# Performance work log

Measured on AMD Instinct MI355X. Metric: run time of the kernel, lower is better.

The kernel has to match this reference:

```python
import jax, jax.numpy as jnp
import numpy as np

C = 512
C8 = C // 8   # query/key dim = 64
C2 = C // 2   # value dim = 256


def setup_inputs() -> dict:
    key = jax.random.key(0)
    ks = jax.random.split(key, 10)
    B, H, W = 4, 64, 64
    x = jax.random.normal(ks[0], (B, H, W, C), dtype=jnp.float32)
    # 1x1 conv kernels expressed as [in_ch, out_ch] matrices + biases
    Wf = jax.random.normal(ks[1], (C, C8), dtype=jnp.float32) * 0.02
    bf = jnp.zeros((C8,), dtype=jnp.float32)
    Wg = jax.random.normal(ks[2], (C, C8), dtype=jnp.float32) * 0.02
    bg = jnp.zeros((C8,), dtype=jnp.float32)
    Wh = jax.random.normal(ks[3], (C, C2), dtype=jnp.float32) * 0.02
    bh = jnp.zeros((C2,), dtype=jnp.float32)
    Wo = jax.random.normal(ks[4], (C2, C), dtype=jnp.float32) * 0.02
    bo = jnp.zeros((C,), dtype=jnp.float32)
    gamma = jax.random.normal(ks[5], (1,), dtype=jnp.float32) * 0.05
    return {"x": x, "Wf": Wf, "bf": bf, "Wg": Wg, "bg": bg,
            "Wh": Wh, "bh": bh, "Wo": Wo, "bo": bo, "gamma": gamma}


def reference(x, Wf, bf, Wg, bg, Wh, bh, Wo, bo, gamma):
    B, H, W, _ = x.shape
    N = H * W
    xf = x.reshape(B, N, C)                               # flatten spatial dims
    f = xf @ Wf + bf                                      # [B, N, C8] keys
    g = xf @ Wg + bg                                      # [B, N, C8] queries
    h = xf @ Wh + bh                                      # [B, N, C2] values
    s = jnp.einsum('bnd,bmd->bnm', g, f)                  # [B, N, N] scores (g @ f^T)
    beta = jax.nn.softmax(s, axis=-1)                     # attention map
    o = jnp.einsum('bnm,bmd->bnd', beta, h)               # [B, N, C2]
    o = o @ Wo + bo                                       # [B, N, C] output 1x1 conv
    out = gamma * o + xf                                  # residual with learned scale
    return out.reshape(B, H, W, C)
```

## Files before the change

kernel.cpp:

```cpp
#include <hip/hip_runtime.h>
#include <math.h>

#define B_   4
#define N_   4096
#define C_   512
#define C8_  64
#define C2_  256
#define LOG2E 1.4426950408889634f

typedef __attribute__((ext_vector_type(8))) short bf16x8;
typedef __attribute__((ext_vector_type(4))) short bf16x4;
typedef __attribute__((ext_vector_type(4))) float floatx4;
typedef __attribute__((ext_vector_type(16))) float floatx16;
typedef __attribute__((ext_vector_type(2))) unsigned uint32x2;

__device__ __forceinline__ short f2bf(float x) {
    unsigned u = __float_as_uint(x);
    u += 0x7fff + ((u >> 16) & 1);
    return (short)(u >> 16);
}
__device__ __forceinline__ unsigned cvtpk(float a, float b) {
    unsigned r;
    asm("v_cvt_pk_bf16_f32 %0, %1, %2" : "=v"(r) : "v"(a), "v"(b));
    return r;
}
__device__ __forceinline__ float bf2f(short s) {
    return __uint_as_float(((unsigned)(unsigned short)s) << 16);
}

union U8 { bf16x8 v; unsigned u[4]; };
union U4 { bf16x4 v; unsigned u[2]; };

__global__ __launch_bounds__(256) void convert_w(
    const float* __restrict__ Wf, const float* __restrict__ Wg,
    const float* __restrict__ Wh, const float* __restrict__ Wo,
    short* __restrict__ WcatT, short* __restrict__ WoT)
{
    int tid = blockIdx.x * 256 + threadIdx.x;
    if (tid < 384 * 512) {
        int n = tid >> 9, k = tid & 511;
        float v = (n < 64)  ? Wf[k * 64 + n]
                : (n < 128) ? Wg[k * 64 + (n - 64)]
                            : Wh[k * 256 + (n - 128)];
        WcatT[tid] = f2bf(v);
    } else {
        int t2 = tid - 384 * 512;
        int n = t2 >> 8, k = t2 & 255;
        WoT[t2] = f2bf(Wo[k * 512 + n]);
    }
}

__global__ __launch_bounds__(256, 3) void qkv_mfma(
    const float* __restrict__ x, const short* __restrict__ WcatT,
    const float* __restrict__ bfv, const float* __restrict__ bgv,
    const float* __restrict__ bhv,
    short* __restrict__ fbf, short* __restrict__ gbf, short* __restrict__ hT)
{
    const int ny = blockIdx.x;
    const int m0 = blockIdx.y * 64;
    const int n0 = ny * 128;
    const int t  = threadIdx.x;
    const int w  = t >> 6, lane = t & 63;
    const int l15 = lane & 15, quad = lane >> 4;
    const int wm = w & 1, wn = w >> 1;

    __shared__ short As[64 * 40];
    __shared__ short Bs[128 * 40];

    const int arow = t >> 2, ako = (t & 3) * 8;

    floatx4 acc[2][4];
    #pragma unroll
    for (int i = 0; i < 2; i++)
        #pragma unroll
        for (int j = 0; j < 4; j++) acc[i][j] = (floatx4){0.f,0.f,0.f,0.f};

    for (int k0 = 0; k0 < C_; k0 += 32) {
        {
            const float* xp = &x[(size_t)(m0 + arow) * C_ + k0 + ako];
            float4 v0 = *(const float4*)xp;
            float4 v1 = *(const float4*)(xp + 4);
            U8 ua;
            ua.u[0] = cvtpk(v0.x, v0.y); ua.u[1] = cvtpk(v0.z, v0.w);
            ua.u[2] = cvtpk(v1.x, v1.y); ua.u[3] = cvtpk(v1.z, v1.w);
            *(bf16x8*)&As[arow * 40 + ako] = ua.v;
        }
        #pragma unroll
        for (int i = 0; i < 2; i++) {
            int c = t + i * 256;
            int nr = c >> 2, ko = (c & 3) * 8;
            *(bf16x8*)&Bs[nr * 40 + ko] =
                *(const bf16x8*)&WcatT[(size_t)(n0 + nr) * 512 + k0 + ko];
        }
        __syncthreads();

        bf16x8 af[2], bfr[4];
        #pragma unroll
        for (int mt = 0; mt < 2; mt++)
            af[mt] = *(const bf16x8*)&As[(wm * 32 + mt * 16 + l15) * 40 + quad * 8];
        #pragma unroll
        for (int nt = 0; nt < 4; nt++)
            bfr[nt] = *(const bf16x8*)&Bs[(wn * 64 + nt * 16 + l15) * 40 + quad * 8];
        #pragma unroll
        for (int mt = 0; mt < 2; mt++)
            #pragma unroll
            for (int nt = 0; nt < 4; nt++)
                acc[mt][nt] = __builtin_amdgcn_mfma_f32_16x16x32_bf16(af[mt], bfr[nt], acc[mt][nt], 0, 0, 0);
        __syncthreads();
    }

    if (ny == 0) {
        #pragma unroll
        for (int mt = 0; mt < 2; mt++) {
            #pragma unroll
            for (int nt = 0; nt < 4; nt++) {
                int cn = wn * 64 + nt * 16 + l15;
                #pragma unroll
                for (int rg = 0; rg < 4; rg++) {
                    int row = m0 + wm * 32 + mt * 16 + quad * 4 + rg;
                    float v = acc[mt][nt][rg];
                    if (cn < 64) fbf[(size_t)row * 64 + cn]        = f2bf(v + bfv[cn]);
                    else         gbf[(size_t)row * 64 + (cn - 64)] = f2bf((v + bgv[cn - 64]) * LOG2E);
                }
            }
        }
    } else {
        #pragma unroll
        for (int mt = 0; mt < 2; mt++) {
            #pragma unroll
            for (int nt = 0; nt < 4; nt++) {
                int hch = (ny - 1) * 128 + wn * 64 + nt * 16 + l15;
                int row = m0 + wm * 32 + mt * 16 + quad * 4;
                int bb = row >> 12, n = row & 4095;
                float bias = bhv[hch];
                U4 pk;
                pk.u[0] = cvtpk(acc[mt][nt][0] + bias, acc[mt][nt][1] + bias);
                pk.u[1] = cvtpk(acc[mt][nt][2] + bias, acc[mt][nt][3] + bias);
                *(bf16x4*)&hT[((size_t)(bb * 256 + hch)) * 4096 + n] = pk.v;
            }
        }
    }
}

#define HST 40

__global__ __launch_bounds__(256, 2) void attn_v6(
    const short* __restrict__ fK,
    const short* __restrict__ gQ,
    const short* __restrict__ hT,
    short* __restrict__ oPart,
    float* __restrict__ lPart,
    int sbits)
{
    const int bx = blockIdx.x;
    const int s  = bx & ((1 << sbits) - 1);
    const int vh = (bx >> sbits) & 1;
    const int qt = (bx >> (sbits + 1)) & 31;
    const int b  = bx >> (sbits + 6);
    const int kb = s << (12 - sbits);
    const int niter = 64 >> sbits;
    const int t  = threadIdx.x;
    const int w  = t >> 6, lane = t & 63;
    const int l31 = lane & 31, h = lane >> 5;
    const int q_wave = qt * 128 + w * 32;

    __shared__ short fs[2][64 * HST];
    __shared__ short hs[2][128 * HST];

    bf16x8 qf[4];
    #pragma unroll
    for (int k = 0; k < 4; k++)
        qf[k] = *(const bf16x8*)&gQ[(size_t)(b * N_ + q_wave + l31) * 64 + k * 16 + h * 8];

    floatx16 oacc[4];
    #pragma unroll
    for (int vt = 0; vt < 4; vt++)
        #pragma unroll
        for (int j = 0; j < 16; j++) oacc[vt][j] = 0.f;
    float lsum = 0.f;

    const int f_row = t >> 2, f_c = (t & 3) * 16;
    const int h_row = t >> 3, h_c = (t & 7) * 8;

    {
        *(bf16x8*)&fs[0][f_row * HST + f_c] =
            *(const bf16x8*)&fK[(size_t)(b * N_ + kb + f_row) * 64 + f_c];
        *(bf16x8*)&fs[0][f_row * HST + f_c + 8] =
            *(const bf16x8*)&fK[(size_t)(b * N_ + kb + f_row) * 64 + f_c + 8];
        #pragma unroll
        for (int i = 0; i < 4; i++)
            *(bf16x8*)&hs[0][(h_row + i * 32) * HST + h_c] =
                *(const bf16x8*)&hT[((size_t)(b * 256 + vh * 128 + h_row + i * 32)) * 4096 + kb + h_c];
    }
    __syncthreads();

    for (int it = 0; it < niter; ++it) {
        const int cur = it & 1;
        const bool more = (it < niter - 1);
        const int kn = kb + (it + 1) * 64;

        bf16x8 rf0, rf1, rh[4];
        if (more) {
            rf0 = *(const bf16x8*)&fK[(size_t)(b * N_ + kn + f_row) * 64 + f_c];
            rf1 = *(const bf16x8*)&fK[(size_t)(b * N_ + kn + f_row) * 64 + f_c + 8];
            #pragma unroll
            for (int i = 0; i < 4; i++)
                rh[i] = *(const bf16x8*)&hT[((size_t)(b * 256 + vh * 128 + h_row + i * 32)) * 4096 + kn + h_c];
        }

        bf16x8 ffr[2][4];
        #pragma unroll
        for (int m = 0; m < 2; m++)
            #pragma unroll
            for (int k = 0; k < 4; k++)
                ffr[m][k] = *(const bf16x8*)&fs[cur][(m * 32 + l31) * HST + k * 16 + h * 8];

        floatx16 sacc[2];
        __builtin_amdgcn_s_setprio(1);
        #pragma unroll
        for (int m = 0; m < 2; m++) {
            #pragma unroll
            for (int j = 0; j < 16; j++) sacc[m][j] = 0.f;
            #pragma unroll
            for (int k = 0; k < 4; k++)
                sacc[m] = __builtin_amdgcn_mfma_f32_32x32x16_bf16(
                    ffr[m][k], qf[k], sacc[m], 0, 0, 0);
        }
        __builtin_amdgcn_s_setprio(0);

        bf16x8 pfrag[4];
        #pragma unroll
        for (int m = 0; m < 2; m++) {
            float p[16]; float ps_ = 0.f;
            #pragma unroll
            for (int j = 0; j < 16; j++) {
                p[j] = __builtin_amdgcn_exp2f(sacc[m][j]);
                ps_ += p[j];
            }
            ps_ += __shfl_xor(ps_, 32);
            lsum += ps_;
            unsigned pk[8];
            #pragma unroll
            for (int i = 0; i < 8; i++) pk[i] = cvtpk(p[2 * i], p[2 * i + 1]);
            #pragma unroll
            for (int kp = 0; kp < 2; kp++) {
                uint32x2 r0 = __builtin_amdgcn_permlane32_swap(pk[4 * kp],     pk[4 * kp + 2], false, false);
                uint32x2 r1 = __builtin_amdgcn_permlane32_swap(pk[4 * kp + 1], pk[4 * kp + 3], false, false);
                U8 u; u.u[0] = r0[0]; u.u[1] = r1[0]; u.u[2] = r0[1]; u.u[3] = r1[1];
                pfrag[m * 2 + kp] = u.v;
            }
        }

        __builtin_amdgcn_s_setprio(1);
        #pragma unroll
        for (int kk2 = 0; kk2 < 4; kk2++)
            #pragma unroll
            for (int vt = 0; vt < 4; vt++) {
                bf16x8 vfr = *(const bf16x8*)&hs[cur][(vt * 32 + l31) * HST + kk2 * 16 + h * 8];
                oacc[vt] = __builtin_amdgcn_mfma_f32_32x32x16_bf16(
                    pfrag[kk2], vfr, oacc[vt], 0, 0, 0);
            }
        __builtin_amdgcn_s_setprio(0);

        if (more) {
            const int nxt = cur ^ 1;
            *(bf16x8*)&fs[nxt][f_row * HST + f_c] = rf0;
            *(bf16x8*)&fs[nxt][f_row * HST + f_c + 8] = rf1;
            #pragma unroll
            for (int i = 0; i < 4; i++)
                *(bf16x8*)&hs[nxt][(h_row + i * 32) * HST + h_c] = rh[i];
        }
        __syncthreads();
    }

    #pragma unroll
    for (int vt = 0; vt < 4; vt++) {
        int vch = vh * 128 + vt * 32 + l31;
        #pragma unroll
        for (int r = 0; r < 16; r++) {
            int q = q_wave + (r & 3) + 8 * (r >> 2) + 4 * h;
            oPart[(size_t)s * 4194304 + (size_t)(b * N_ + q) * 256 + vch] = f2bf(oacc[vt][r]);
        }
    }
    if (vh == 0 && lane < 32)
        lPart[(size_t)s * 16384 + b * N_ + q_wave + lane] = lsum;
}

__global__ __launch_bounds__(256, 2) void out_mfma(
    const short* __restrict__ oPart, const float* __restrict__ lPart,
    const short* __restrict__ WoT,
    const float* __restrict__ bo, const float* __restrict__ x,
    const float* __restrict__ gamma, float* __restrict__ out)
{
    const int n0 = blockIdx.x * 256;
    const int m0 = blockIdx.y * 64;
    const int t  = threadIdx.x;
    const int w  = t >> 6, lane = t & 63;
    const int l15 = lane & 15, quad = lane >> 4;
    const int wm = w & 1, wn = w >> 1;

    __shared__ short As[64 * 40];
    __shared__ short Bs[256 * 40];
    __shared__ float linv[64];

    if (t < 64)
        linv[t] = 1.0f / (lPart[m0 + t] + lPart[16384 + m0 + t]);

    const int arow = t >> 2, ako = (t & 3) * 8;

    floatx4 acc[2][8];
    #pragma unroll
    for (int i = 0; i < 2; i++)
        #pragma unroll
        for (int j = 0; j < 8; j++) acc[i][j] = (floatx4){0.f,0.f,0.f,0.f};

    __syncthreads();

    for (int k0 = 0; k0 < C2_; k0 += 32) {
        {
            size_t gb = (size_t)(m0 + arow) * 256 + k0 + ako;
            bf16x8 o0 = *(const bf16x8*)&oPart[gb];
            bf16x8 o1 = *(const bf16x8*)&oPart[4194304 + gb];
            float li = linv[arow];
            U8 u;
            #pragma unroll
            for (int j = 0; j < 4; j++) {
                float a0 = (bf2f(o0[2 * j])     + bf2f(o1[2 * j]))     * li;
                float a1 = (bf2f(o0[2 * j + 1]) + bf2f(o1[2 * j + 1])) * li;
                u.u[j] = cvtpk(a0, a1);
            }
            *(bf16x8*)&As[arow * 40 + ako] = u.v;
        }
        #pragma unroll
        for (int i = 0; i < 4; i++) {
            int c = t + i * 256;
            int nr = c >> 2, ko = (c & 3) * 8;
            *(bf16x8*)&Bs[nr * 40 + ko] =
                *(const bf16x8*)&WoT[(size_t)(n0 + nr) * 256 + k0 + ko];
        }
        __syncthreads();

        bf16x8 af[2], bfr[8];
        #pragma unroll
        for (int mt = 0; mt < 2; mt++)
            af[mt] = *(const bf16x8*)&As[(wm * 32 + mt * 16 + l15) * 40 + quad * 8];
        #pragma unroll
        for (int nt = 0; nt < 8; nt++)
            bfr[nt] = *(const bf16x8*)&Bs[(wn * 128 + nt * 16 + l15) * 40 + quad * 8];
        #pragma unroll
        for (int mt = 0; mt < 2; mt++)
            #pragma unroll
            for (int nt = 0; nt < 8; nt++)
                acc[mt][nt] = __builtin_amdgcn_mfma_f32_16x16x32_bf16(af[mt], bfr[nt], acc[mt][nt], 0, 0, 0);
        __syncthreads();
    }

    const float gm = gamma[0];
    #pragma unroll
    for (int mt = 0; mt < 2; mt++) {
        #pragma unroll
        for (int nt = 0; nt < 8; nt++) {
            int col = n0 + wn * 128 + nt * 16 + l15;
            float bias = bo[col];
            #pragma unroll
            for (int rg = 0; rg < 4; rg++) {
                int row = m0 + wm * 32 + mt * 16 + quad * 4 + rg;
                out[(size_t)row * C_ + col] =
                    gm * (acc[mt][nt][rg] + bias) + x[(size_t)row * C_ + col];
            }
        }
    }
}

extern "C" void kernel_launch(void* const* d_in, const int* in_sizes, int n_in,
                              void* d_out, int out_size, void* d_ws, size_t ws_size,
                              hipStream_t stream) {
    (void)in_sizes; (void)n_in; (void)out_size; (void)ws_size;

    const float* x     = (const float*)d_in[0];
    const float* Wf    = (const float*)d_in[1];
    const float* bfv   = (const float*)d_in[2];
    const float* Wg    = (const float*)d_in[3];
    const float* bgv   = (const float*)d_in[4];
    const float* Wh    = (const float*)d_in[5];
    const float* bhv   = (const float*)d_in[6];
    const float* Wo    = (const float*)d_in[7];
    const float* bo    = (const float*)d_in[8];
    const float* gamma = (const float*)d_in[9];
    float* out = (float*)d_out;

    short* fbf   = (short*)d_ws;
    short* gbf   = fbf   + (size_t)B_ * N_ * C8_;
    short* hT    = gbf   + (size_t)B_ * N_ * C8_;
    short* WcatT = hT    + (size_t)B_ * C2_ * N_;
    short* WoT   = WcatT + (size_t)384 * 512;
    short* oPart = WoT   + (size_t)512 * 256;
    float* lPart = (float*)(oPart + (size_t)2 * 16384 * 256);

    const int sbits = 1;

    convert_w<<<1280, 256, 0, stream>>>(Wf, Wg, Wh, Wo, WcatT, WoT);
    qkv_mfma<<<dim3(3, 256), 256, 0, stream>>>(x, WcatT, bfv, bgv, bhv, fbf, gbf, hT);
    attn_v6<<<256 << sbits, 256, 0, stream>>>(fbf, gbf, hT, oPart, lPart, sbits);
    out_mfma<<<dim3(2, 256), 256, 0, stream>>>(oPart, lPart, WoT, bo, x, gamma, out);
}
```

Before: 194.4 us.

## Single-buffer attention LDS, raise occupancy, and split keys four ways

The attention kernel drops the double-buffered LDS (the two buffer slots are reused as the two halves of the key dimension) and adds an extra barrier before the shared-memory writes. It also restructures the score loop to process one 32-row block at a time so fewer registers are live, and raises launch bounds to 3 blocks per CU. The key-split factor goes from 2 to 4, and the output projection now sums a variable number of partial outputs and row sums. This trades lost load/compute overlap and a second barrier per iteration for higher occupancy and more blocks, while the output kernel reads twice as much partial data.

```diff
diff --git a/kernel.cpp b/kernel.cpp
--- a/kernel.cpp
+++ b/kernel.cpp
@@ -143,8 +143,10 @@
 }
 
 #define HST 40
-
-__global__ __launch_bounds__(256, 2) void attn_v6(
+#define FS_H (64 * HST + 32)
+#define HS_H (128 * HST + 32)
+
+__global__ __launch_bounds__(256, 3) void attn_v9(
     const short* __restrict__ fK,
     const short* __restrict__ gQ,
     const short* __restrict__ hT,
@@ -164,8 +166,8 @@
     const int l31 = lane & 31, h = lane >> 5;
     const int q_wave = qt * 128 + w * 32;
 
-    __shared__ short fs[2][64 * HST];
-    __shared__ short hs[2][128 * HST];
+    __shared__ short fs[2][FS_H];
+    __shared__ short hs[2][HS_H];
 
     bf16x8 qf[4];
     #pragma unroll
@@ -180,22 +182,23 @@
     float lsum = 0.f;
 
     const int f_row = t >> 2, f_c = (t & 3) * 16;
+    const int fh = f_c >> 5, fw = f_c & 31;
     const int h_row = t >> 3, h_c = (t & 7) * 8;
+    const int hh = h_c >> 5, hw = h_c & 31;
 
     {
-        *(bf16x8*)&fs[0][f_row * HST + f_c] =
+        *(bf16x8*)&fs[fh][f_row * HST + fw] =
             *(const bf16x8*)&fK[(size_t)(b * N_ + kb + f_row) * 64 + f_c];
-        *(bf16x8*)&fs[0][f_row * HST + f_c + 8] =
+        *(bf16x8*)&fs[fh][f_row * HST + fw + 8] =
             *(const bf16x8*)&fK[(size_t)(b * N_ + kb + f_row) * 64 + f_c + 8];
         #pragma unroll
         for (int i = 0; i < 4; i++)
-            *(bf16x8*)&hs[0][(h_row + i * 32) * HST + h_c] =
+            *(bf16x8*)&hs[hh][(h_row + i * 32) * HST + hw] =
                 *(const bf16x8*)&hT[((size_t)(b * 256 + vh * 128 + h_row + i * 32)) * 4096 + kb + h_c];
     }
     __syncthreads();
 
     for (int it = 0; it < niter; ++it) {
-        const int cur = it & 1;
         const bool more = (it < niter - 1);
         const int kn = kb + (it + 1) * 64;
 
@@ -208,33 +211,27 @@
                 rh[i] = *(const bf16x8*)&hT[((size_t)(b * 256 + vh * 128 + h_row + i * 32)) * 4096 + kn + h_c];
         }
 
-        bf16x8 ffr[2][4];
-        #pragma unroll
-        for (int m = 0; m < 2; m++)
+        bf16x8 pfrag[4];
+        #pragma unroll
+        for (int m = 0; m < 2; m++) {
+            bf16x8 ffr[4];
             #pragma unroll
             for (int k = 0; k < 4; k++)
-                ffr[m][k] = *(const bf16x8*)&fs[cur][(m * 32 + l31) * HST + k * 16 + h * 8];
-
-        floatx16 sacc[2];
-        __builtin_amdgcn_s_setprio(1);
-        #pragma unroll
-        for (int m = 0; m < 2; m++) {
-            #pragma unroll
-            for (int j = 0; j < 16; j++) sacc[m][j] = 0.f;
+                ffr[k] = *(const bf16x8*)&fs[k >> 1][(m * 32 + l31) * HST + (k & 1) * 16 + h * 8];
+
+            floatx16 sacc;
+            #pragma unroll
+            for (int j = 0; j < 16; j++) sacc[j] = 0.f;
+            __builtin_amdgcn_s_setprio(1);
             #pragma unroll
             for (int k = 0; k < 4; k++)
-                sacc[m] = __builtin_amdgcn_mfma_f32_32x32x16_bf16(
-                    ffr[m][k], qf[k], sacc[m], 0, 0, 0);
-        }
-        __builtin_amdgcn_s_setprio(0);
-
-        bf16x8 pfrag[4];
-        #pragma unroll
-        for (int m = 0; m < 2; m++) {
+                sacc = __builtin_amdgcn_mfma_f32_32x32x16_bf16(ffr[k], qf[k], sacc, 0, 0, 0);
+            __builtin_amdgcn_s_setprio(0);
+
             float p[16]; float ps_ = 0.f;
             #pragma unroll
             for (int j = 0; j < 16; j++) {
-                p[j] = __builtin_amdgcn_exp2f(sacc[m][j]);
+                p[j] = __builtin_amdgcn_exp2f(sacc[j]);
                 ps_ += p[j];
             }
             ps_ += __shfl_xor(ps_, 32);
@@ -256,21 +253,21 @@
         for (int kk2 = 0; kk2 < 4; kk2++)
             #pragma unroll
             for (int vt = 0; vt < 4; vt++) {
-                bf16x8 vfr = *(const bf16x8*)&hs[cur][(vt * 32 + l31) * HST + kk2 * 16 + h * 8];
+                bf16x8 vfr = *(const bf16x8*)&hs[kk2 >> 1][(vt * 32 + l31) * HST + (kk2 & 1) * 16 + h * 8];
                 oacc[vt] = __builtin_amdgcn_mfma_f32_32x32x16_bf16(
                     pfrag[kk2], vfr, oacc[vt], 0, 0, 0);
             }
         __builtin_amdgcn_s_setprio(0);
 
+        __syncthreads();
         if (more) {
-            const int nxt = cur ^ 1;
-            *(bf16x8*)&fs[nxt][f_row * HST + f_c] = rf0;
-            *(bf16x8*)&fs[nxt][f_row * HST + f_c + 8] = rf1;
+            *(bf16x8*)&fs[fh][f_row * HST + fw] = rf0;
+            *(bf16x8*)&fs[fh][f_row * HST + fw + 8] = rf1;
             #pragma unroll
             for (int i = 0; i < 4; i++)
-                *(bf16x8*)&hs[nxt][(h_row + i * 32) * HST + h_c] = rh[i];
-        }
-        __syncthreads();
+                *(bf16x8*)&hs[hh][(h_row + i * 32) * HST + hw] = rh[i];
+            __syncthreads();
+        }
     }
 
     #pragma unroll
@@ -290,7 +287,8 @@
     const short* __restrict__ oPart, const float* __restrict__ lPart,
     const short* __restrict__ WoT,
     const float* __restrict__ bo, const float* __restrict__ x,
-    const float* __restrict__ gamma, float* __restrict__ out)
+    const float* __restrict__ gamma, float* __restrict__ out,
+    int nsplit)
 {
     const int n0 = blockIdx.x * 256;
     const int m0 = blockIdx.y * 64;
@@ -303,8 +301,11 @@
     __shared__ short Bs[256 * 40];
     __shared__ float linv[64];
 
-    if (t < 64)
-        linv[t] = 1.0f / (lPart[m0 + t] + lPart[16384 + m0 + t]);
+    if (t < 64) {
+        float l = 0.f;
+        for (int s2 = 0; s2 < nsplit; s2++) l += lPart[(size_t)s2 * 16384 + m0 + t];
+        linv[t] = 1.0f / l;
+    }
 
     const int arow = t >> 2, ako = (t & 3) * 8;
 
@@ -319,16 +320,19 @@
     for (int k0 = 0; k0 < C2_; k0 += 32) {
         {
             size_t gb = (size_t)(m0 + arow) * 256 + k0 + ako;
-            bf16x8 o0 = *(const bf16x8*)&oPart[gb];
-            bf16x8 o1 = *(const bf16x8*)&oPart[4194304 + gb];
+            float a[8];
+            #pragma unroll
+            for (int j = 0; j < 8; j++) a[j] = 0.f;
+            for (int s2 = 0; s2 < nsplit; s2++) {
+                bf16x8 o = *(const bf16x8*)&oPart[(size_t)s2 * 4194304 + gb];
+                #pragma unroll
+                for (int j = 0; j < 8; j++) a[j] += bf2f(o[j]);
+            }
             float li = linv[arow];
             U8 u;
             #pragma unroll
-            for (int j = 0; j < 4; j++) {
-                float a0 = (bf2f(o0[2 * j])     + bf2f(o1[2 * j]))     * li;
-                float a1 = (bf2f(o0[2 * j + 1]) + bf2f(o1[2 * j + 1])) * li;
-                u.u[j] = cvtpk(a0, a1);
-            }
+            for (int j = 0; j < 4; j++)
+                u.u[j] = cvtpk(a[2 * j] * li, a[2 * j + 1] * li);
             *(bf16x8*)&As[arow * 40 + ako] = u.v;
         }
         #pragma unroll
@@ -395,12 +399,12 @@
     short* WcatT = hT    + (size_t)B_ * C2_ * N_;
     short* WoT   = WcatT + (size_t)384 * 512;
     short* oPart = WoT   + (size_t)512 * 256;
-    float* lPart = (float*)(oPart + (size_t)2 * 16384 * 256);
-
-    const int sbits = 1;
+    float* lPart = (float*)(oPart + (size_t)4 * 16384 * 256);
+
+    const int sbits = 2;
 
     convert_w<<<1280, 256, 0, stream>>>(Wf, Wg, Wh, Wo, WcatT, WoT);
     qkv_mfma<<<dim3(3, 256), 256, 0, stream>>>(x, WcatT, bfv, bgv, bhv, fbf, gbf, hT);
-    attn_v6<<<256 << sbits, 256, 0, stream>>>(fbf, gbf, hT, oPart, lPart, sbits);
-    out_mfma<<<dim3(2, 256), 256, 0, stream>>>(oPart, lPart, WoT, bo, x, gamma, out);
-}
+    attn_v9<<<256 << sbits, 256, 0, stream>>>(fbf, gbf, hT, oPart, lPart, sbits);
+    out_mfma<<<dim3(2, 256), 256, 0, stream>>>(oPart, lPart, WoT, bo, x, gamma, out, 1 << sbits);
+}
```

Measured after the change: 204.4 us. +5.2%, slower.
